# Kernel tuning notes

Hardware: AMD Instinct MI355X
Metric: run time of the kernel (lower is better)

The kernel has to match this reference:

```python
import jax, jax.numpy as jnp
import numpy as np

N, C, R, P1, P2 = 8, 3, 8, 512, 512
EPS = 1e-10


def setup_inputs() -> dict:
    key = jax.random.key(0)
    k1, k2, k3, k4 = jax.random.split(key, 4)
    X = jax.random.uniform(k1, (N, C, P1, P2), dtype=jnp.float32)
    S = jax.random.uniform(k2, (C, R), dtype=jnp.float32)
    # mimic the learned-init normalization: unit-norm columns of S
    S = S / jnp.linalg.norm(S, axis=0, keepdims=True)
    gamma = jax.random.uniform(k3, (1,), dtype=jnp.float32) * 1e-5
    lam = jax.random.uniform(k4, (1,), dtype=jnp.float32) * 1e-5
    return {"X": X, "S": S, "gamma": gamma, "lam": lam, "n_iter": 3}


def reference(X, S, gamma, lam, n_iter):
    n, c, p1, p2 = X.shape
    r = S.shape[1]
    p = p1 * p2
    X = X.reshape(n, c, p)
    gamma = jnp.abs(gamma)  # (1,)
    lam = jnp.abs(lam)      # (1,)
    Dt = jnp.zeros((n, r, p), dtype=X.dtype)
    x0 = jnp.mean(X, axis=2, keepdims=True)
    for _ in range(n_iter):
        # ---- D update (proximal gradient) ----
        SDt = jnp.einsum('cr,nrp->ncp', S, Dt)                    # [n,c,p]
        x0 = jnp.mean(X + SDt, axis=2, keepdims=True)             # [n,c,1]
        tau_D = 1.0 / jnp.sum(S * S)                              # 1/||S||_F^2
        Dt = Dt - tau_D * (jnp.einsum('cr,ncp->nrp', S, SDt + X)
                           - jnp.einsum('cr,ncq->nrq', S, x0))
        S_nrm = jnp.linalg.norm(S, axis=0).reshape(1, r, 1)       # col L2 norms of S
        Dt = jax.nn.relu(Dt - lam * gamma * tau_D * S_nrm)        # L1 prox
        Dt_L2 = jnp.linalg.norm(Dt, axis=2, keepdims=True)        # [n,r,1]
        scl = jax.nn.relu(Dt_L2 - lam * tau_D * S_nrm)
        scl = scl / Dt_L2 + EPS                                   # faithful to source
        Dt = Dt * scl                                             # L2 (group) prox
        # ---- S update (proximal gradient) ----
        SDt = jnp.einsum('cr,nrp->ncp', S, Dt)
        x0 = jnp.mean(X + SDt, axis=2, keepdims=True)             # [n,c,1]
        Dt_sum = jnp.sum(Dt, axis=2, keepdims=True)               # [n,r,1]
        tau_S = 1.0 / jnp.mean(jnp.sum(Dt * Dt, axis=(1, 2)))     # 1/mean ||Dt_i||_F^2
        G = (jnp.einsum('ncp,nrp->ncr', SDt + X, Dt)
             - x0 @ jnp.swapaxes(Dt_sum, 1, 2))                   # [n,c,r]
        S_grad = S - tau_S * jnp.mean(G, axis=0)                  # [c,r]
        Dt_nrm = jnp.mean(gamma * jnp.sum(jnp.abs(Dt), axis=2, keepdims=True)
                          + jnp.linalg.norm(Dt, axis=2, keepdims=True), axis=0)  # [r,1]
        S_nrm2 = jnp.linalg.norm(S_grad, axis=0, keepdims=True)   # [1,r]
        scl_S = jax.nn.relu(S_nrm2 - lam * tau_S * Dt_nrm.T)
        scl_S = scl_S / (S_nrm2 + EPS)
        S = S_grad * scl_S
        # ---- unit-norm rescaling of S columns ----
        S_nrm3 = jnp.linalg.norm(S, axis=0, keepdims=True)        # [1,r]
        S = S / (S_nrm3 + EPS)
        Dt = Dt * (S_nrm3.reshape(1, r, 1) + EPS)
    return (x0, S, Dt.reshape(n, r, p1, p2))
```

## Files before the change

### kernel.cpp

```cpp
#include <hip/hip_runtime.h>
#include <math.h>

#define N_ 8
#define C_ 3
#define R_ 8
#define P_ 262144
#define EPS_ 1e-10f
#define INVP_ (1.0f / (float)P_)
#define NRED 68

#define WS_S      0
#define WS_GAMMA  24
#define WS_LAM    25
#define WS_TAUD   26
#define WS_ALPHA  32
#define WS_MEANX  96
#define WS_B      120
#define WS_THRESH 184
#define WS_RED    192
#define WS_END    736

__global__ void k_init(float* __restrict__ ws, const float* __restrict__ S_in,
                       const float* __restrict__ gamma, const float* __restrict__ lam) {
    int t = threadIdx.x;
    if (t < 24) ws[WS_S + t] = S_in[t];
    if (t == 24) ws[WS_GAMMA] = fabsf(gamma[0]);
    if (t == 25) ws[WS_LAM]   = fabsf(lam[0]);
    for (int i = WS_ALPHA + t; i < WS_END; i += (int)blockDim.x) ws[i] = 0.0f;
}

__global__ void k_meanX(const float* __restrict__ X, float* __restrict__ ws) {
    const int slice = blockIdx.y;
    const float4* Xv = (const float4*)(X + (size_t)slice * P_);
    int tid  = blockIdx.x * blockDim.x + threadIdx.x;
    int nthr = gridDim.x * blockDim.x;
    float s = 0.f;
    for (int i = tid; i < P_ / 4; i += nthr) {
        float4 v = Xv[i];
        s += v.x + v.y + v.z + v.w;
    }
    for (int off = 32; off; off >>= 1) s += __shfl_down(s, off);
    __shared__ float lds[4];
    int lane = threadIdx.x & 63, wv = threadIdx.x >> 6;
    if (lane == 0) lds[wv] = s;
    __syncthreads();
    if (threadIdx.x == 0) {
        float t = lds[0] + lds[1] + lds[2] + lds[3];
        atomicAdd(&ws[WS_MEANX + slice], t);
    }
}

__global__ __launch_bounds__(64) void k_preD(float* __restrict__ ws) {
    const int lane = threadIdx.x;
    const int r = lane & 7, n = lane >> 3;
    __shared__ float sS[C_][R_];
    __shared__ float sMx[N_][C_];
    if (lane < 24) {
        float v = ws[WS_MEANX + lane] * INVP_;
        ws[WS_MEANX + lane] = v;
        sMx[lane / C_][lane % C_] = v;
    }
    if (lane < 24) sS[lane / R_][lane % R_] = ws[WS_S + lane];
    const float gamma = ws[WS_GAMMA], lam = ws[WS_LAM];
    __syncthreads();
    float ss = 0.f;
    for (int c = 0; c < C_; ++c)
        for (int rr = 0; rr < R_; ++rr) ss += sS[c][rr] * sS[c][rr];
    float tauD = 1.0f / ss;
    if (lane == 0) ws[WS_TAUD] = tauD;
    if (n == 0) {
        float sn = sqrtf(sS[0][r]*sS[0][r] + sS[1][r]*sS[1][r] + sS[2][r]*sS[2][r]);
        ws[WS_THRESH + r] = lam * gamma * tauD * sn;
    }
    float b = 0.f;
    for (int c = 0; c < C_; ++c) b += sS[c][r] * sMx[n][c];
    ws[WS_B + lane] = b;
}

__global__ __launch_bounds__(256) void k_pass(const float* __restrict__ X,
                                              float* __restrict__ Dt,
                                              float* __restrict__ ws, int first) {
    const int n = blockIdx.y;
    float S[C_][R_], al[R_], bb[R_], th[R_];
#pragma unroll
    for (int c = 0; c < C_; ++c)
#pragma unroll
        for (int r = 0; r < R_; ++r) S[c][r] = ws[WS_S + c * R_ + r];
#pragma unroll
    for (int r = 0; r < R_; ++r) {
        al[r] = ws[WS_ALPHA + n * R_ + r];
        bb[r] = ws[WS_B + n * R_ + r];
        th[r] = ws[WS_THRESH + r];
    }
    const float tauD = ws[WS_TAUD];

    const float4* Xv = (const float4*)(X + (size_t)n * C_ * P_);
    float4* Dv = (float4*)(Dt + (size_t)n * R_ * P_);
    const int P4 = P_ / 4;

    float acc[NRED];
#pragma unroll
    for (int k = 0; k < NRED; ++k) acc[k] = 0.f;

    int tid  = blockIdx.x * blockDim.x + threadIdx.x;
    int nthr = gridDim.x * blockDim.x;
    for (int i = tid; i < P4; i += nthr) {
        float4 xq[C_];
#pragma unroll
        for (int c = 0; c < C_; ++c) xq[c] = Xv[(size_t)c * P4 + i];
        float4 dq[R_];
        if (!first) {
#pragma unroll
            for (int r = 0; r < R_; ++r) dq[r] = Dv[(size_t)r * P4 + i];
        }
        float4 wq[R_];
#pragma unroll
        for (int j = 0; j < 4; ++j) {
            float ts[C_];
#pragma unroll
            for (int c = 0; c < C_; ++c) ts[c] = ((const float*)&xq[c])[j];
            float v[R_];
#pragma unroll
            for (int r = 0; r < R_; ++r) {
                v[r] = first ? 0.f : al[r] * ((const float*)&dq[r])[j];
#pragma unroll
                for (int c = 0; c < C_; ++c) ts[c] += S[c][r] * v[r];
            }
#pragma unroll
            for (int r = 0; r < R_; ++r) {
                float g = S[0][r] * ts[0] + S[1][r] * ts[1] + S[2][r] * ts[2] - bb[r];
                float u = v[r] - tauD * g - th[r];
                ((float*)&wq[r])[j] = fmaxf(u, 0.f);
            }
        }
#pragma unroll
        for (int r = 0; r < R_; ++r) Dv[(size_t)r * P4 + i] = wq[r];
#pragma unroll
        for (int r = 0; r < R_; ++r)
            acc[r] += wq[r].x + wq[r].y + wq[r].z + wq[r].w;
#pragma unroll
        for (int r = 0; r < R_; ++r)
#pragma unroll
            for (int r2 = 0; r2 <= r; ++r2)
                acc[8 + (r * (r + 1)) / 2 + r2] +=
                    wq[r].x * wq[r2].x + wq[r].y * wq[r2].y + wq[r].z * wq[r2].z + wq[r].w * wq[r2].w;
#pragma unroll
        for (int c = 0; c < C_; ++c)
#pragma unroll
            for (int r = 0; r < R_; ++r)
                acc[44 + c * R_ + r] +=
                    xq[c].x * wq[r].x + xq[c].y * wq[r].y + xq[c].z * wq[r].z + xq[c].w * wq[r].w;
    }

    __shared__ float lds[4][NRED];
    int lane = threadIdx.x & 63, wv = threadIdx.x >> 6;
#pragma unroll
    for (int k = 0; k < NRED; ++k) {
        float s = acc[k];
        for (int off = 32; off; off >>= 1) s += __shfl_down(s, off);
        if (lane == 0) lds[wv][k] = s;
    }
    __syncthreads();
    if (threadIdx.x < NRED) {
        float s = lds[0][threadIdx.x] + lds[1][threadIdx.x] + lds[2][threadIdx.x] + lds[3][threadIdx.x];
        atomicAdd(&ws[WS_RED + n * NRED + threadIdx.x], s);
    }
}

__global__ __launch_bounds__(64) void k_post(float* __restrict__ ws, float* __restrict__ out) {
    const int lane = threadIdx.x;
    const int r = lane & 7, n = lane >> 3;
    __shared__ float sS[C_][R_];
    __shared__ float sMx[N_][C_];
    __shared__ float sSumD[N_][R_];
    __shared__ float sGm[N_][R_][R_ + 1];
    __shared__ float sXd[N_][C_][R_];
    __shared__ float sScl[N_][R_];
    __shared__ float sX0[N_][C_];
    __shared__ float sSf[C_][R_];
    __shared__ float sAl[N_][R_];

    const float gamma = ws[WS_GAMMA], lam = ws[WS_LAM], tauD = ws[WS_TAUD];

    if (lane < 24) sS[lane / R_][lane % R_] = ws[WS_S + lane];
    if (lane < 24) sMx[lane / C_][lane % C_] = ws[WS_MEANX + lane];
    const float* red = ws + WS_RED + n * NRED;
    const float sumD = red[r];
    sSumD[n][r] = sumD;
#pragma unroll
    for (int r2 = 0; r2 < R_; ++r2) {
        int hi = r > r2 ? r : r2, lo = r + r2 - hi;
        sGm[n][r][r2] = red[8 + (hi * (hi + 1)) / 2 + lo];
    }
#pragma unroll
    for (int c = 0; c < C_; ++c) sXd[n][c][r] = red[44 + c * R_ + r];
    __syncthreads();

    const float snrm = sqrtf(sS[0][r]*sS[0][r] + sS[1][r]*sS[1][r] + sS[2][r]*sS[2][r]);
    const float Gdiag = sGm[n][r][r];
    const float L2 = sqrtf(Gdiag);
    const float sc = fmaxf(L2 - lam * tauD * snrm, 0.f) / L2 + EPS_;
    sScl[n][r] = sc;
    float ssq = sc * sc * Gdiag;
#pragma unroll
    for (int m = 1; m < 64; m <<= 1) ssq += __shfl_xor(ssq, m);
    float dtn = gamma * sc * sumD + sc * L2;
#pragma unroll
    for (int m = 8; m < 64; m <<= 1) dtn += __shfl_xor(dtn, m);
    __syncthreads();

    if (lane < N_ * C_) {
        int n2 = lane / C_, c2 = lane % C_;
        float x0 = sMx[n2][c2];
#pragma unroll
        for (int rr = 0; rr < R_; ++rr)
            x0 += sS[c2][rr] * sScl[n2][rr] * sSumD[n2][rr] * INVP_;
        sX0[n2][c2] = x0;
        out[lane] = x0;
    }
    __syncthreads();

    float Gc[C_];
#pragma unroll
    for (int c = 0; c < C_; ++c) {
        float t = 0.f;
#pragma unroll
        for (int r2 = 0; r2 < R_; ++r2)
            t += sS[c][r2] * sScl[n][r2] * sGm[n][r2][r];
        float G = t * sc + sc * sXd[n][c][r] - sX0[n][c] * sc * sumD;
#pragma unroll
        for (int m = 8; m < 64; m <<= 1) G += __shfl_xor(G, m);
        Gc[c] = G;
    }
    const float tauS = (float)N_ / ssq;
    float Sg[C_];
#pragma unroll
    for (int c = 0; c < C_; ++c) Sg[c] = sS[c][r] - tauS * (Gc[c] / (float)N_);
    const float sn2 = sqrtf(Sg[0]*Sg[0] + Sg[1]*Sg[1] + Sg[2]*Sg[2]);
    const float Dn = dtn / (float)N_;
    const float ssS = fmaxf(sn2 - lam * tauS * Dn, 0.f) / (sn2 + EPS_);
    float s1[C_];
#pragma unroll
    for (int c = 0; c < C_; ++c) s1[c] = Sg[c] * ssS;
    const float sn3 = sqrtf(s1[0]*s1[0] + s1[1]*s1[1] + s1[2]*s1[2]);
    float Sf[C_];
#pragma unroll
    for (int c = 0; c < C_; ++c) Sf[c] = s1[c] / (sn3 + EPS_);
    const float alpha = sc * (sn3 + EPS_);
    ws[WS_ALPHA + lane] = alpha;
    sAl[n][r] = alpha;
    if (n == 0) {
#pragma unroll
        for (int c = 0; c < C_; ++c) {
            ws[WS_S + c * R_ + r] = Sf[c];
            out[24 + c * R_ + r] = Sf[c];
            sSf[c][r] = Sf[c];
        }
    }
    float p2 = Sf[0]*Sf[0] + Sf[1]*Sf[1] + Sf[2]*Sf[2];
#pragma unroll
    for (int m = 1; m < 8; m <<= 1) p2 += __shfl_xor(p2, m);
    const float tauD2 = 1.0f / p2;
    if (lane == 0) ws[WS_TAUD] = tauD2;
    if (n == 0) {
        float snf = sqrtf(Sf[0]*Sf[0] + Sf[1]*Sf[1] + Sf[2]*Sf[2]);
        ws[WS_THRESH + r] = lam * gamma * tauD2 * snf;
    }
    __syncthreads();

    float b = 0.f;
#pragma unroll
    for (int c = 0; c < C_; ++c) {
        float x0n = sMx[n][c];
#pragma unroll
        for (int rr = 0; rr < R_; ++rr)
            x0n += sSf[c][rr] * sAl[n][rr] * sSumD[n][rr] * INVP_;
        b += sSf[c][r] * x0n;
    }
    ws[WS_B + lane] = b;
    for (int i = lane; i < N_ * NRED; i += 64) ws[WS_RED + i] = 0.f;
}

__global__ __launch_bounds__(256) void k_final(float* __restrict__ Dt, const float* __restrict__ ws) {
    const int nr = blockIdx.y;
    const float a = ws[WS_ALPHA + nr];
    float4* Dv = (float4*)(Dt + (size_t)nr * P_);
    int tid  = blockIdx.x * blockDim.x + threadIdx.x;
    int nthr = gridDim.x * blockDim.x;
    for (int i = tid; i < P_ / 4; i += nthr) {
        float4 v = Dv[i];
        v.x *= a; v.y *= a; v.z *= a; v.w *= a;
        Dv[i] = v;
    }
}

extern "C" void kernel_launch(void* const* d_in, const int* in_sizes, int n_in,
                              void* d_out, int out_size, void* d_ws, size_t ws_size,
                              hipStream_t stream) {
    const float* X     = (const float*)d_in[0];
    const float* S_in  = (const float*)d_in[1];
    const float* gamma = (const float*)d_in[2];
    const float* lam   = (const float*)d_in[3];

    float* out = (float*)d_out;
    float* ws  = (float*)d_ws;
    float* Dt  = out + 48;

    k_init<<<1, 256, 0, stream>>>(ws, S_in, gamma, lam);
    k_meanX<<<dim3(64, N_ * C_), 256, 0, stream>>>(X, ws);
    k_preD<<<1, 64, 0, stream>>>(ws);
    for (int it = 0; it < 3; ++it) {
        k_pass<<<dim3(64, N_), 256, 0, stream>>>(X, Dt, ws, it == 0 ? 1 : 0);
        k_post<<<1, 64, 0, stream>>>(ws, out);
    }
    k_final<<<dim3(64, N_ * R_), 256, 0, stream>>>(Dt, ws);
}
```

Baseline: 243.2 us.

## Fuse all iterations into one cooperative kernel keeping Dt in registers

```diff
diff --git a/kernel.cpp b/kernel.cpp
--- a/kernel.cpp
+++ b/kernel.cpp
@@ -1,13 +1,319 @@
 #include <hip/hip_runtime.h>
+#include <hip/hip_cooperative_groups.h>
 #include <math.h>
 
 #define N_ 8
 #define C_ 3
 #define R_ 8
 #define P_ 262144
+#define P4_ 65536
 #define EPS_ 1e-10f
 #define INVP_ (1.0f / (float)P_)
 #define NRED 68
+
+#define CB_  256
+#define BPN_ 32
+#define CH4_ 2048
+#define JCH  8
+
+#define WC_MEANX 0
+#define WC_RED   32
+#define WC_ZEND  (32 + 3 * N_ * NRED)
+
+namespace cg = cooperative_groups;
+
+__global__ void k_zero(float* __restrict__ ws) {
+    int t = blockIdx.x * blockDim.x + threadIdx.x;
+    if (t < WC_ZEND) ws[t] = 0.f;
+}
+
+__global__ __launch_bounds__(256, 1) void k_all(
+    const float* __restrict__ X, const float* __restrict__ S_in,
+    const float* __restrict__ gammap, const float* __restrict__ lamp,
+    float* __restrict__ out, float* __restrict__ ws)
+{
+    cg::grid_group grid = cg::this_grid();
+    const int t    = threadIdx.x;
+    const int blk  = blockIdx.x;
+    const int n    = blk >> 5;
+    const int bblk = blk & 31;
+    const int lane = t & 63, wv = t >> 6;
+    const int r_l  = t & 7, n_l = (t >> 3) & 7;
+
+    __shared__ float lds[4][NRED];
+    __shared__ float sS[C_][R_];
+    __shared__ float sMx[N_][C_];
+    __shared__ float sTh[R_];
+    __shared__ float sB[N_][R_];
+    __shared__ float sAl[N_][R_];
+    __shared__ float sSumD[N_][R_];
+    __shared__ float sGm[N_][R_][R_ + 1];
+    __shared__ float sXd[N_][C_][R_];
+    __shared__ float sScl[N_][R_];
+    __shared__ float sX0[N_][C_];
+    __shared__ float sTau[1];
+
+    const float gamma = fabsf(gammap[0]);
+    const float lam   = fabsf(lamp[0]);
+    const float4* X4  = (const float4*)X;
+
+    float pc[C_];
+#pragma unroll
+    for (int c = 0; c < C_; ++c) {
+        float s = 0.f;
+#pragma unroll
+        for (int j = 0; j < JCH; ++j) {
+            float4 v = X4[(size_t)(n * C_ + c) * P4_ + bblk * CH4_ + j * 256 + t];
+            s += v.x + v.y + v.z + v.w;
+        }
+        pc[c] = s;
+    }
+    if (t < 24) sS[t / R_][t % R_] = S_in[t];
+#pragma unroll
+    for (int c = 0; c < C_; ++c) {
+        float s = pc[c];
+        for (int off = 32; off; off >>= 1) s += __shfl_down(s, off);
+        if (lane == 0) lds[wv][c] = s;
+    }
+    __syncthreads();
+    if (t < C_)
+        atomicAdd(&ws[WC_MEANX + n * C_ + t],
+                  lds[0][t] + lds[1][t] + lds[2][t] + lds[3][t]);
+    grid.sync();
+
+    if (t < 24) sMx[t / C_][t % C_] = ws[WC_MEANX + t] * INVP_;
+    __syncthreads();
+    {
+        float ss = 0.f;
+#pragma unroll
+        for (int c = 0; c < C_; ++c)
+#pragma unroll
+            for (int rr = 0; rr < R_; ++rr) ss += sS[c][rr] * sS[c][rr];
+        float tauD0 = 1.f / ss;
+        if (t == 0) sTau[0] = tauD0;
+        if (t < R_) {
+            float sn = sqrtf(sS[0][t]*sS[0][t] + sS[1][t]*sS[1][t] + sS[2][t]*sS[2][t]);
+            sTh[t] = lam * gamma * tauD0 * sn;
+        }
+        if (t < 64) {
+            float b = 0.f;
+#pragma unroll
+            for (int c = 0; c < C_; ++c) b += sS[c][r_l] * sMx[n_l][c];
+            sB[n_l][r_l] = b;
+            sAl[n_l][r_l] = 0.f;
+        }
+    }
+    __syncthreads();
+
+    float4 dt[R_][JCH];
+#pragma unroll
+    for (int rr = 0; rr < R_; ++rr)
+#pragma unroll
+        for (int j = 0; j < JCH; ++j) dt[rr][j] = make_float4(0.f, 0.f, 0.f, 0.f);
+
+    for (int it = 0; it < 3; ++it) {
+        float Sreg[C_][R_], al[R_], bbr[R_], thr[R_];
+#pragma unroll
+        for (int c = 0; c < C_; ++c)
+#pragma unroll
+            for (int rr = 0; rr < R_; ++rr) Sreg[c][rr] = sS[c][rr];
+#pragma unroll
+        for (int rr = 0; rr < R_; ++rr) {
+            al[rr] = sAl[n][rr]; bbr[rr] = sB[n][rr]; thr[rr] = sTh[rr];
+        }
+        const float tauD = sTau[0];
+        float accS[R_], accG[36];
+#pragma unroll
+        for (int k = 0; k < R_; ++k) accS[k] = 0.f;
+#pragma unroll
+        for (int k = 0; k < 36; ++k) accG[k] = 0.f;
+
+#pragma unroll
+        for (int j = 0; j < JCH; ++j) {
+            float4 xq0 = X4[(size_t)(n * C_ + 0) * P4_ + bblk * CH4_ + j * 256 + t];
+            float4 xq1 = X4[(size_t)(n * C_ + 1) * P4_ + bblk * CH4_ + j * 256 + t];
+            float4 xq2 = X4[(size_t)(n * C_ + 2) * P4_ + bblk * CH4_ + j * 256 + t];
+#pragma unroll
+            for (int q = 0; q < 4; ++q) {
+                float ts0 = ((float*)&xq0)[q], ts1 = ((float*)&xq1)[q], ts2 = ((float*)&xq2)[q];
+                float v[R_];
+#pragma unroll
+                for (int rr = 0; rr < R_; ++rr) {
+                    v[rr] = al[rr] * ((float*)&dt[rr][j])[q];
+                    ts0 += Sreg[0][rr] * v[rr];
+                    ts1 += Sreg[1][rr] * v[rr];
+                    ts2 += Sreg[2][rr] * v[rr];
+                }
+#pragma unroll
+                for (int rr = 0; rr < R_; ++rr) {
+                    float g = Sreg[0][rr]*ts0 + Sreg[1][rr]*ts1 + Sreg[2][rr]*ts2 - bbr[rr];
+                    float u = v[rr] - tauD * g - thr[rr];
+                    ((float*)&dt[rr][j])[q] = fmaxf(u, 0.f);
+                }
+            }
+#pragma unroll
+            for (int rr = 0; rr < R_; ++rr) {
+                float4 w = dt[rr][j];
+                accS[rr] += w.x + w.y + w.z + w.w;
+#pragma unroll
+                for (int r2 = 0; r2 <= rr; ++r2) {
+                    float4 w2 = dt[r2][j];
+                    accG[(rr*(rr+1))/2 + r2] += w.x*w2.x + w.y*w2.y + w.z*w2.z + w.w*w2.w;
+                }
+            }
+        }
+
+        float accX[C_][R_];
+#pragma unroll
+        for (int c = 0; c < C_; ++c)
+#pragma unroll
+            for (int rr = 0; rr < R_; ++rr) accX[c][rr] = 0.f;
+#pragma unroll
+        for (int j = 0; j < JCH; ++j) {
+            float4 xq0 = X4[(size_t)(n * C_ + 0) * P4_ + bblk * CH4_ + j * 256 + t];
+            float4 xq1 = X4[(size_t)(n * C_ + 1) * P4_ + bblk * CH4_ + j * 256 + t];
+            float4 xq2 = X4[(size_t)(n * C_ + 2) * P4_ + bblk * CH4_ + j * 256 + t];
+#pragma unroll
+            for (int rr = 0; rr < R_; ++rr) {
+                float4 w = dt[rr][j];
+                accX[0][rr] += xq0.x*w.x + xq0.y*w.y + xq0.z*w.z + xq0.w*w.w;
+                accX[1][rr] += xq1.x*w.x + xq1.y*w.y + xq1.z*w.z + xq1.w*w.w;
+                accX[2][rr] += xq2.x*w.x + xq2.y*w.y + xq2.z*w.z + xq2.w*w.w;
+            }
+        }
+
+        __syncthreads();
+        float* redit = ws + WC_RED + (size_t)(it * N_ + n) * NRED;
+#pragma unroll
+        for (int k = 0; k < NRED; ++k) {
+            float s = (k < 8) ? accS[k] : (k < 44 ? accG[k - 8] : accX[(k - 44) / R_][(k - 44) % R_]);
+            for (int off = 32; off; off >>= 1) s += __shfl_down(s, off);
+            if (lane == 0) lds[wv][k] = s;
+        }
+        __syncthreads();
+        if (t < NRED)
+            atomicAdd(&redit[t], lds[0][t] + lds[1][t] + lds[2][t] + lds[3][t]);
+        grid.sync();
+
+        if (t < 64) {
+            const float* red = ws + WC_RED + (size_t)(it * N_ + n_l) * NRED;
+            sSumD[n_l][r_l] = red[r_l];
+#pragma unroll
+            for (int r2 = 0; r2 < R_; ++r2) {
+                int hi = r_l > r2 ? r_l : r2, lo = r_l + r2 - hi;
+                sGm[n_l][r_l][r2] = red[8 + (hi*(hi+1))/2 + lo];
+            }
+#pragma unroll
+            for (int c = 0; c < C_; ++c) sXd[n_l][c][r_l] = red[44 + c * R_ + r_l];
+        }
+        __syncthreads();
+
+        float sc = 0.f, ssq = 0.f, dtn = 0.f, sumD = 0.f;
+        if (t < 64) {
+            sumD = sSumD[n_l][r_l];
+            const float tauDc = sTau[0];
+            const float snrm = sqrtf(sS[0][r_l]*sS[0][r_l] + sS[1][r_l]*sS[1][r_l] + sS[2][r_l]*sS[2][r_l]);
+            const float Gdiag = sGm[n_l][r_l][r_l];
+            const float L2 = sqrtf(Gdiag);
+            sc = fmaxf(L2 - lam * tauDc * snrm, 0.f) / L2 + EPS_;
+            sScl[n_l][r_l] = sc;
+            ssq = sc * sc * Gdiag;
+#pragma unroll
+            for (int m = 1; m < 64; m <<= 1) ssq += __shfl_xor(ssq, m);
+            dtn = gamma * sc * sumD + sc * L2;
+#pragma unroll
+            for (int m = 8; m < 64; m <<= 1) dtn += __shfl_xor(dtn, m);
+        }
+        __syncthreads();
+
+        if (t < N_ * C_) {
+            int n2 = t / C_, c2 = t % C_;
+            float x0 = sMx[n2][c2];
+#pragma unroll
+            for (int rr = 0; rr < R_; ++rr)
+                x0 += sS[c2][rr] * sScl[n2][rr] * sSumD[n2][rr] * INVP_;
+            sX0[n2][c2] = x0;
+            if (blk == 0) out[t] = x0;
+        }
+        __syncthreads();
+
+        float Sf[C_] = {0.f, 0.f, 0.f};
+        float alpha = 0.f, tauDn = 0.f;
+        if (t < 64) {
+            float Gc[C_];
+#pragma unroll
+            for (int c = 0; c < C_; ++c) {
+                float tt = 0.f;
+#pragma unroll
+                for (int r2 = 0; r2 < R_; ++r2)
+                    tt += sS[c][r2] * sScl[n_l][r2] * sGm[n_l][r2][r_l];
+                float G = tt * sc + sc * sXd[n_l][c][r_l] - sX0[n_l][c] * sc * sumD;
+#pragma unroll
+                for (int m = 8; m < 64; m <<= 1) G += __shfl_xor(G, m);
+                Gc[c] = G;
+            }
+            const float tauS = (float)N_ / ssq;
+            float Sg[C_];
+#pragma unroll
+            for (int c = 0; c < C_; ++c) Sg[c] = sS[c][r_l] - tauS * (Gc[c] / (float)N_);
+            const float sn2 = sqrtf(Sg[0]*Sg[0] + Sg[1]*Sg[1] + Sg[2]*Sg[2]);
+            const float Dn = dtn / (float)N_;
+            const float ssS = fmaxf(sn2 - lam * tauS * Dn, 0.f) / (sn2 + EPS_);
+            float s1[C_];
+#pragma unroll
+            for (int c = 0; c < C_; ++c) s1[c] = Sg[c] * ssS;
+            const float sn3 = sqrtf(s1[0]*s1[0] + s1[1]*s1[1] + s1[2]*s1[2]);
+#pragma unroll
+            for (int c = 0; c < C_; ++c) Sf[c] = s1[c] / (sn3 + EPS_);
+            alpha = sc * (sn3 + EPS_);
+            float p2 = Sf[0]*Sf[0] + Sf[1]*Sf[1] + Sf[2]*Sf[2];
+#pragma unroll
+            for (int m = 1; m < 8; m <<= 1) p2 += __shfl_xor(p2, m);
+            tauDn = 1.f / p2;
+        }
+        __syncthreads();
+        if (t < 64) {
+            sAl[n_l][r_l] = alpha;
+            if (n_l == 0) {
+#pragma unroll
+                for (int c = 0; c < C_; ++c) {
+                    sS[c][r_l] = Sf[c];
+                    if (blk == 0) out[24 + c * R_ + r_l] = Sf[c];
+                }
+                const float snf = sqrtf(Sf[0]*Sf[0] + Sf[1]*Sf[1] + Sf[2]*Sf[2]);
+                sTh[r_l] = lam * gamma * tauDn * snf;
+            }
+            if (t == 0) sTau[0] = tauDn;
+        }
+        __syncthreads();
+        if (t < 64) {
+            float b = 0.f;
+#pragma unroll
+            for (int c = 0; c < C_; ++c) {
+                float x0n = sMx[n_l][c];
+#pragma unroll
+                for (int rr = 0; rr < R_; ++rr)
+                    x0n += sS[c][rr] * sAl[n_l][rr] * sSumD[n_l][rr] * INVP_;
+                b += sS[c][r_l] * x0n;
+            }
+            sB[n_l][r_l] = b;
+        }
+        __syncthreads();
+    }
+
+    float4* O4 = (float4*)(out + 48);
+#pragma unroll
+    for (int rr = 0; rr < R_; ++rr) {
+        const float a = sAl[n][rr];
+        float4* o = O4 + (size_t)(n * R_ + rr) * P4_ + bblk * CH4_ + t;
+#pragma unroll
+        for (int j = 0; j < JCH; ++j) {
+            float4 v = dt[rr][j];
+            v.x *= a; v.y *= a; v.z *= a; v.w *= a;
+            o[j * 256] = v;
+        }
+    }
+}
 
 #define WS_S      0
 #define WS_GAMMA  24
@@ -32,7 +338,7 @@
 __global__ void k_meanX(const float* __restrict__ X, float* __restrict__ ws) {
     const int slice = blockIdx.y;
     const float4* Xv = (const float4*)(X + (size_t)slice * P_);
-    int tid  = blockIdx.x * blockDim.x + threadIdx.x;
+    int tid = blockIdx.x * blockDim.x + threadIdx.x;
     int nthr = gridDim.x * blockDim.x;
     float s = 0.f;
     for (int i = tid; i < P_ / 4; i += nthr) {
@@ -44,10 +350,8 @@
     int lane = threadIdx.x & 63, wv = threadIdx.x >> 6;
     if (lane == 0) lds[wv] = s;
     __syncthreads();
-    if (threadIdx.x == 0) {
-        float t = lds[0] + lds[1] + lds[2] + lds[3];
-        atomicAdd(&ws[WS_MEANX + slice], t);
-    }
+    if (threadIdx.x == 0)
+        atomicAdd(&ws[WS_MEANX + slice], lds[0] + lds[1] + lds[2] + lds[3]);
 }
 
 __global__ __launch_bounds__(64) void k_preD(float* __restrict__ ws) {
@@ -93,16 +397,13 @@
         th[r] = ws[WS_THRESH + r];
     }
     const float tauD = ws[WS_TAUD];
-
     const float4* Xv = (const float4*)(X + (size_t)n * C_ * P_);
     float4* Dv = (float4*)(Dt + (size_t)n * R_ * P_);
     const int P4 = P_ / 4;
-
     float acc[NRED];
 #pragma unroll
     for (int k = 0; k < NRED; ++k) acc[k] = 0.f;
-
-    int tid  = blockIdx.x * blockDim.x + threadIdx.x;
+    int tid = blockIdx.x * blockDim.x + threadIdx.x;
     int nthr = gridDim.x * blockDim.x;
     for (int i = tid; i < P4; i += nthr) {
         float4 xq[C_];
@@ -151,7 +452,6 @@
                 acc[44 + c * R_ + r] +=
                     xq[c].x * wq[r].x + xq[c].y * wq[r].y + xq[c].z * wq[r].z + xq[c].w * wq[r].w;
     }
-
     __shared__ float lds[4][NRED];
     int lane = threadIdx.x & 63, wv = threadIdx.x >> 6;
 #pragma unroll
@@ -179,9 +479,7 @@
     __shared__ float sX0[N_][C_];
     __shared__ float sSf[C_][R_];
     __shared__ float sAl[N_][R_];
-
     const float gamma = ws[WS_GAMMA], lam = ws[WS_LAM], tauD = ws[WS_TAUD];
-
     if (lane < 24) sS[lane / R_][lane % R_] = ws[WS_S + lane];
     if (lane < 24) sMx[lane / C_][lane % C_] = ws[WS_MEANX + lane];
     const float* red = ws + WS_RED + n * NRED;
@@ -195,7 +493,6 @@
 #pragma unroll
     for (int c = 0; c < C_; ++c) sXd[n][c][r] = red[44 + c * R_ + r];
     __syncthreads();
-
     const float snrm = sqrtf(sS[0][r]*sS[0][r] + sS[1][r]*sS[1][r] + sS[2][r]*sS[2][r]);
     const float Gdiag = sGm[n][r][r];
     const float L2 = sqrtf(Gdiag);
@@ -208,7 +505,6 @@
 #pragma unroll
     for (int m = 8; m < 64; m <<= 1) dtn += __shfl_xor(dtn, m);
     __syncthreads();
-
     if (lane < N_ * C_) {
         int n2 = lane / C_, c2 = lane % C_;
         float x0 = sMx[n2][c2];
@@ -219,15 +515,14 @@
         out[lane] = x0;
     }
     __syncthreads();
-
     float Gc[C_];
 #pragma unroll
     for (int c = 0; c < C_; ++c) {
-        float t = 0.f;
+        float tt = 0.f;
 #pragma unroll
         for (int r2 = 0; r2 < R_; ++r2)
-            t += sS[c][r2] * sScl[n][r2] * sGm[n][r2][r];
-        float G = t * sc + sc * sXd[n][c][r] - sX0[n][c] * sc * sumD;
+            tt += sS[c][r2] * sScl[n][r2] * sGm[n][r2][r];
+        float G = tt * sc + sc * sXd[n][c][r] - sX0[n][c] * sc * sumD;
 #pragma unroll
         for (int m = 8; m < 64; m <<= 1) G += __shfl_xor(G, m);
         Gc[c] = G;
@@ -260,14 +555,13 @@
     float p2 = Sf[0]*Sf[0] + Sf[1]*Sf[1] + Sf[2]*Sf[2];
 #pragma unroll
     for (int m = 1; m < 8; m <<= 1) p2 += __shfl_xor(p2, m);
-    const float tauD2 = 1.0f / p2;
-    if (lane == 0) ws[WS_TAUD] = tauD2;
+    const float tauDn = 1.0f / p2;
+    if (lane == 0) ws[WS_TAUD] = tauDn;
     if (n == 0) {
         float snf = sqrtf(Sf[0]*Sf[0] + Sf[1]*Sf[1] + Sf[2]*Sf[2]);
-        ws[WS_THRESH + r] = lam * gamma * tauD2 * snf;
-    }
-    __syncthreads();
-
+        ws[WS_THRESH + r] = lam * gamma * tauDn * snf;
+    }
+    __syncthreads();
     float b = 0.f;
 #pragma unroll
     for (int c = 0; c < C_; ++c) {
@@ -285,7 +579,7 @@
     const int nr = blockIdx.y;
     const float a = ws[WS_ALPHA + nr];
     float4* Dv = (float4*)(Dt + (size_t)nr * P_);
-    int tid  = blockIdx.x * blockDim.x + threadIdx.x;
+    int tid = blockIdx.x * blockDim.x + threadIdx.x;
     int nthr = gridDim.x * blockDim.x;
     for (int i = tid; i < P_ / 4; i += nthr) {
         float4 v = Dv[i];
@@ -304,8 +598,15 @@
 
     float* out = (float*)d_out;
     float* ws  = (float*)d_ws;
-    float* Dt  = out + 48;
-
+
+    k_zero<<<(WC_ZEND + 255) / 256, 256, 0, stream>>>(ws);
+    void* args[] = { (void*)&X, (void*)&S_in, (void*)&gamma, (void*)&lam,
+                     (void*)&out, (void*)&ws };
+    hipError_t err = hipLaunchCooperativeKernel((const void*)k_all, dim3(CB_),
+                                                dim3(256), args, 0, stream);
+    if (err == hipSuccess) return;
+
+    float* Dt = out + 48;
     k_init<<<1, 256, 0, stream>>>(ws, S_in, gamma, lam);
     k_meanX<<<dim3(64, N_ * C_), 256, 0, stream>>>(X, ws);
     k_preD<<<1, 64, 0, stream>>>(ws);
```

Result: slower. 460.8 us (+89.4%).
